# Performance work log

Measured on AMD Instinct MI355X. Metric: run time of the kernel, lower is better.

The kernel has to match this reference:

```python
import jax, jax.numpy as jnp
import numpy as np

C = 80           # foreground classes
B, N = 8, 4000   # images, proposals per image
K_PRE = 2048     # pre-NMS candidates per image (fixed-shape stand-in for torch.where filtering)
DET = 100        # detection_per_image
SCORE_THRESH = 0.01
NMS_THRESH = 0.5
MIN_AREA = 0.1
BBOX_W = (10.0, 10.0, 5.0, 5.0)
CLIP = float(np.log(1000.0 / 16.0))
CLS_OFFSET = 4096.0               # > max image coordinate, for batched (per-class) NMS


def setup_inputs() -> dict:
    key = jax.random.key(0)
    k1, k2, k3, k4 = jax.random.split(key, 4)
    p1 = jax.random.uniform(k1, (B, N, 2)) * 800.0
    wh = jax.random.uniform(k2, (B, N, 2)) * 200.0 + 1.0
    proposals = jnp.concatenate([p1, p1 + wh], axis=-1)          # [B,N,4] x1,y1,x2,y2
    label_pre = jax.random.normal(k3, (B, N, C + 1), dtype=jnp.float32)
    bbox_pre = jax.random.normal(k4, (B, N, (C + 1) * 4), dtype=jnp.float32) * 0.5
    return {"label_pre": label_pre, "bbox_pre": bbox_pre, "proposals": proposals}


def decode_boxes(deltas, props):
    w = props[..., 2] - props[..., 0]
    h = props[..., 3] - props[..., 1]
    cx = props[..., 0] + 0.5 * w
    cy = props[..., 1] + 0.5 * h
    dx = deltas[..., 0] / BBOX_W[0]
    dy = deltas[..., 1] / BBOX_W[1]
    dw = jnp.minimum(deltas[..., 2] / BBOX_W[2], CLIP)
    dh = jnp.minimum(deltas[..., 3] / BBOX_W[3], CLIP)
    pcx = dx * w + cx
    pcy = dy * h + cy
    pw = jnp.exp(dw) * w
    ph = jnp.exp(dh) * h
    return jnp.stack([pcx - 0.5 * pw, pcy - 0.5 * ph,
                      pcx + 0.5 * pw, pcy + 0.5 * ph], axis=-1)


def pairwise_iou(b):
    # b [K,4] -> [K,K]
    area = jnp.maximum(b[:, 2] - b[:, 0], 0.0) * jnp.maximum(b[:, 3] - b[:, 1], 0.0)
    lt = jnp.maximum(b[:, None, :2], b[None, :, :2])
    rb = jnp.minimum(b[:, None, 2:], b[None, :, 2:])
    wh = jnp.maximum(rb - lt, 0.0)
    inter = wh[..., 0] * wh[..., 1]
    union = area[:, None] + area[None, :] - inter
    return inter / jnp.maximum(union, 1e-9)


def greedy_nms_keep(boxes, valid):
    # boxes already sorted by score (descending); returns kept mask
    K = boxes.shape[0]
    iou = pairwise_iou(boxes)
    idx = jnp.arange(K)

    def body(i, keep):
        sup = (iou[i] > NMS_THRESH) & (idx > i) & keep[i]
        return keep & ~sup

    return jax.lax.fori_loop(0, K, body, valid)


def process_image(logits, deltas, props):
    probs = jax.nn.softmax(logits, axis=-1)            # [N, C+1]
    scores = probs[:, 1:].reshape(-1)                  # [N*C]
    d = deltas[:, 4:].reshape(N, C, 4)                 # drop background deltas
    boxes = decode_boxes(d, props[:, None, :]).reshape(-1, 4)   # [N*C, 4]
    labels = jnp.broadcast_to(jnp.arange(1, C + 1), (N, C)).reshape(-1)
    area = (boxes[:, 3] - boxes[:, 1]) * (boxes[:, 2] - boxes[:, 0])
    valid = (scores > SCORE_THRESH) & (area > MIN_AREA)
    masked = jnp.where(valid, scores, -1.0)
    top_scores, top_idx = jax.lax.top_k(masked, K_PRE)
    top_boxes = boxes[top_idx]
    top_labels = labels[top_idx]
    keep0 = top_scores > 0.0
    # batched_nms: per-class coordinate offset so classes never suppress each other
    off = (top_labels.astype(top_boxes.dtype) * CLS_OFFSET)[:, None]
    keep = greedy_nms_keep(top_boxes + off, keep0)
    final = jnp.where(keep, top_scores, -1.0)
    det_scores, det_idx = jax.lax.top_k(final, DET)
    return top_boxes[det_idx], det_scores, top_labels[det_idx]


def reference(label_pre, bbox_pre, proposals):
    # returns (boxes [B,DET,4], scores [B,DET], labels [B,DET]); entries with score<0 are padding
    return jax.vmap(process_image)(label_pre, bbox_pre, proposals)
```

## Files before the change

### kernel.cpp

```cpp
#include <hip/hip_runtime.h>
#include <stdint.h>

#define B_ 8
#define N_ 4000
#define C_ 80
#define NC_ (N_ * C_)
#define KP_ 2048
#define CAND_ 4096
#define SLOTS_ 32
#define SLOTCAP_ 128
#define DET_ 100
#define NW_ 32
#define CLIP_ 4.135166556742356f

#define PB_ 16
#define IB_ (N_ / PB_)
#define CB_ 64
#define FB_ 128
#define NBLK_ ((NC_ / 4 + 255) / 256)

#define RT_ 256
#define RBLK_ (CAND_ / RT_)

typedef unsigned long long u64;

__device__ __forceinline__ void decode4(const float4 pr, const float4 d,
                                        float& x1, float& y1, float& x2, float& y2) {
  float w = pr.z - pr.x, h = pr.w - pr.y;
  float cx = pr.x + 0.5f * w, cy = pr.y + 0.5f * h;
  float dx = d.x / 10.0f, dy = d.y / 10.0f;
  float dw = fminf(d.z / 5.0f, CLIP_), dh = fminf(d.w / 5.0f, CLIP_);
  float pcx = dx * w + cx, pcy = dy * h + cy;
  float pw = expf(dw) * w, ph = expf(dh) * h;
  x1 = pcx - 0.5f * pw; y1 = pcy - 0.5f * ph;
  x2 = pcx + 0.5f * pw; y2 = pcy + 0.5f * ph;
}

__global__ __launch_bounds__(256) void k_scores(const float* __restrict__ logits,
                                                uint32_t* __restrict__ keys,
                                                uint32_t* __restrict__ imgHist) {
  __shared__ float lds[PB_ * 81];
  __shared__ float mArr[PB_], dArr[PB_];
  __shared__ uint32_t hcnt[CB_];
  int blk = blockIdx.x;
  int b = blk / IB_, lb = blk - b * IB_;
  int p0 = b * N_ + lb * PB_;
  int t = threadIdx.x;
  if (t < CB_) hcnt[t] = 0;
  const float4* src = (const float4*)(logits + (size_t)p0 * 81);
  for (int k = t; k < PB_ * 81 / 4; k += 256) ((float4*)lds)[k] = src[k];
  __syncthreads();
  if (t < PB_) {
    const float* lp = lds + t * 81;
    float m = lp[0];
    for (int i = 1; i <= C_; ++i) m = fmaxf(m, lp[i]);
    float denom = 0.f;
    for (int i = 0; i <= C_; ++i) denom += expf(lp[i] - m);
    mArr[t] = m; dArr[t] = denom;
  }
  __syncthreads();
#pragma unroll
  for (int iter = 0; iter < PB_ * C_ / 256; ++iter) {
    int e = iter * 256 + t;
    int pp = e / C_, c = e - pp * C_;
    float lv = lds[pp * 81 + c + 1];
    float score = expf(lv - mArr[pp]) / dArr[pp];
    uint32_t key = 0;
    if (score > 0.01f) {
      key = __float_as_uint(score);
      atomicAdd(&hcnt[(key >> 20) - 960], 1u);
    }
    keys[(size_t)p0 * C_ + e] = key;
  }
  __syncthreads();
  if (t < CB_ && hcnt[t]) atomicAdd(&imgHist[b * CB_ + t], hcnt[t]);
}

__global__ __launch_bounds__(256) void k_refine(const uint32_t* __restrict__ keys,
                                                const uint32_t* __restrict__ imgHist,
                                                uint32_t* __restrict__ fineHist) {
  __shared__ int s_cb;
  int blk = blockIdx.x;
  int b = blk / NBLK_, lb = blk - b * NBLK_;
  int t = threadIdx.x;
  if (t < 64) {
    uint32_t v = imgHist[b * CB_ + t];
#pragma unroll
    for (int d = 1; d < 64; d <<= 1) {
      uint32_t o = __shfl_down(v, d);
      v += (t + d < 64) ? o : 0;
    }
    uint32_t nxt = __shfl_down(v, 1);
    if (t == 63) nxt = 0;
    uint32_t total = __shfl(v, 0);
    if (t == 0 && total < KP_) s_cb = -1;
    if (total >= KP_ && v >= KP_ && nxt < KP_) s_cb = t;
  }
  __syncthreads();
  int cb = s_cb;
  if (cb < 0) return;
  int ti = lb * 256 + t;
  if (ti >= NC_ / 4) return;
  uint4 k4 = ((const uint4*)(keys + (size_t)b * NC_))[ti];
  uint32_t want = (uint32_t)(cb + 960);
  uint32_t kv[4] = {k4.x, k4.y, k4.z, k4.w};
#pragma unroll
  for (int q = 0; q < 4; ++q)
    if ((kv[q] >> 20) == want)
      atomicAdd(&fineHist[b * FB_ + ((kv[q] >> 13) & (FB_ - 1))], 1u);
}

__global__ __launch_bounds__(256) void k_compact(const uint32_t* __restrict__ keys,
                                                 const uint32_t* __restrict__ imgHist,
                                                 const uint32_t* __restrict__ fineHist,
                                                 uint32_t* __restrict__ cnt,
                                                 u64* __restrict__ cand) {
  __shared__ int s_cb;
  __shared__ uint32_t s_tail;
  __shared__ uint32_t s_thr;
  int blk = blockIdx.x;
  int b = blk / NBLK_, lb = blk - b * NBLK_;
  int t = threadIdx.x;
  if (t < 64) {
    uint32_t v = imgHist[b * CB_ + t];
#pragma unroll
    for (int d = 1; d < 64; d <<= 1) {
      uint32_t o = __shfl_down(v, d);
      v += (t + d < 64) ? o : 0;
    }
    uint32_t nxt = __shfl_down(v, 1);
    if (t == 63) nxt = 0;
    uint32_t total = __shfl(v, 0);
    if (t == 0 && total < KP_) { s_cb = -1; s_tail = 0; }
    if (total >= KP_ && v >= KP_ && nxt < KP_) { s_cb = t; s_tail = nxt; }
  }
  __syncthreads();
  int cb = s_cb;
  if (cb < 0) {
    if (t == 0) s_thr = 1u;
  } else if (t < 64) {
    uint32_t f0 = fineHist[b * FB_ + 2 * t];
    uint32_t f1 = fineHist[b * FB_ + 2 * t + 1];
    uint32_t v = f0 + f1;
#pragma unroll
    for (int d = 1; d < 64; d <<= 1) {
      uint32_t o = __shfl_down(v, d);
      v += (t + d < 64) ? o : 0;
    }
    uint32_t nxt = __shfl_down(v, 1);
    if (t == 63) nxt = 0;
    uint32_t tail = s_tail;
    bool c0 = (tail + v >= KP_);
    bool c1 = (tail + nxt + f1 >= KP_);
    bool cN = (tail + nxt >= KP_);
    if (c0 && !c1) s_thr = ((uint32_t)(cb + 960) << 20) | ((uint32_t)(2 * t) << 13);
    if (c1 && !cN) s_thr = ((uint32_t)(cb + 960) << 20) | ((uint32_t)(2 * t + 1) << 13);
  }
  __syncthreads();
  uint32_t thrb = s_thr;
  int ti = lb * 256 + t;
  if (ti >= NC_ / 4) return;
  uint4 k4 = ((const uint4*)(keys + (size_t)b * NC_))[ti];
  int slot = (ti >> 4) & (SLOTS_ - 1);
  uint32_t kv[4] = {k4.x, k4.y, k4.z, k4.w};
  int ns = 0;
#pragma unroll
  for (int q = 0; q < 4; ++q) ns += (kv[q] >= thrb) ? 1 : 0;
  if (ns == 0) return;
  uint32_t pos = atomicAdd(&cnt[(b * SLOTS_ + slot) * 16], (uint32_t)ns);
  u64* seg = cand + (size_t)b * CAND_ + slot * SLOTCAP_;
  uint32_t baseIdx = (uint32_t)(ti * 4);
#pragma unroll
  for (int q = 0; q < 4; ++q) {
    if (kv[q] >= thrb) {
      if (pos < SLOTCAP_)
        seg[pos] = ((u64)kv[q] << 32) | (uint32_t)(~(baseIdx + q));
      ++pos;
    }
  }
}

__global__ __launch_bounds__(256) void k_rank_topk(
    const u64* __restrict__ cand,
    const float* __restrict__ bbox, const float* __restrict__ props,
    float* __restrict__ topScore, int* __restrict__ topLabel,
    float* __restrict__ topBox, float* __restrict__ nmsBox) {
  __shared__ u64 sh[CAND_];
  int blk = blockIdx.x;
  int b = blk / RBLK_, lb = blk - b * RBLK_;
  int t = threadIdx.x;
  const u64* cb2 = cand + (size_t)b * CAND_;
  for (int k = t; k < CAND_ / 2; k += RT_)
    ((ulonglong2*)sh)[k] = ((const ulonglong2*)cb2)[k];
  u64 ki = cb2[lb * RT_ + t];
  __syncthreads();
  int cnt = 0;
#pragma unroll 8
  for (int j = 0; j < CAND_; j += 2) {
    u64 a = sh[j];
    u64 c2 = sh[j + 1];
    cnt += (a > ki) ? 1 : 0;
    cnt += (c2 > ki) ? 1 : 0;
  }
  if (ki != 0ull && cnt < KP_) {
    uint32_t sbits = (uint32_t)(ki >> 32);
    uint32_t idx = ~((uint32_t)ki);
    int n = idx / C_, c = idx % C_;
    float4 pr4 = ((const float4*)props)[(size_t)b * N_ + n];
    float4 d = ((const float4*)(bbox + ((size_t)b * N_ + n) * ((C_ + 1) * 4)))[c + 1];
    float x1, y1, x2, y2;
    decode4(pr4, d, x1, y1, x2, y2);
    float off = (float)(c + 1) * 4096.0f;
    size_t o = (size_t)b * KP_ + (size_t)cnt;
    topScore[o] = __uint_as_float(sbits);
    topLabel[o] = c + 1;
    ((float4*)topBox)[o] = make_float4(x1, y1, x2, y2);
    ((float4*)nmsBox)[o] = make_float4(x1 + off, y1 + off, x2 + off, y2 + off);
  }
}

__global__ __launch_bounds__(64) void k_supmat(const float* __restrict__ nmsBox,
                                               u64* __restrict__ sup) {
  int blk = blockIdx.x;
  int b = blk / 528, r = blk - b * 528;
  int ti = 0, rem = r;
  while (rem >= 32 - ti) { rem -= 32 - ti; ++ti; }
  int tj = ti + rem;
  __shared__ float4 shj[64];
  __shared__ float sha[64];
  int l = threadIdx.x;
  const float4* boxes = (const float4*)(nmsBox + (size_t)b * KP_ * 4);
  float4 bj0 = boxes[tj * 64 + l];
  shj[l] = bj0;
  sha[l] = fmaxf(bj0.z - bj0.x, 0.f) * fmaxf(bj0.w - bj0.y, 0.f);
  int i = ti * 64 + l;
  float4 bi = boxes[i];
  float areai = fmaxf(bi.z - bi.x, 0.f) * fmaxf(bi.w - bi.y, 0.f);
  __syncthreads();
  u64 bits = 0;
  for (int jj = 0; jj < 64; ++jj) {
    int j = tj * 64 + jj;
    if (j > i) {
      float4 bj = shj[jj];
      float ltx = fmaxf(bi.x, bj.x), lty = fmaxf(bi.y, bj.y);
      float rbx = fminf(bi.z, bj.z), rby = fminf(bi.w, bj.w);
      float iw = fmaxf(rbx - ltx, 0.f), ih = fmaxf(rby - lty, 0.f);
      float inter = iw * ih;
      float uni = areai + sha[jj] - inter;
      float iou = inter / fmaxf(uni, 1e-9f);
      if (iou > 0.5f) bits |= (1ull << jj);
    }
  }
  sup[((size_t)b * KP_ + i) * NW_ + tj] = bits;
}

__global__ __launch_bounds__(64) void k_nms_scan(const u64* __restrict__ sup,
                                                 const float* __restrict__ topScore,
                                                 const int* __restrict__ topLabel,
                                                 const float* __restrict__ topBox,
                                                 float* __restrict__ out) {
  int b = blockIdx.x, l = threadIdx.x;
  int h = l >> 5, w = l & 31;
  const u64* base = sup + (size_t)b * KP_ * NW_;
  const float* ts = topScore + (size_t)b * KP_;
  const int* tl = topLabel + (size_t)b * KP_;
  const float4* tb = (const float4*)(topBox + (size_t)b * KP_ * 4);
  unsigned m32 = 0;
#pragma unroll
  for (int j = 0; j < 8; ++j) {
    float4 s4 = ((const float4*)ts)[l * 8 + j];
    if (!(s4.x > 0.f)) m32 |= 1u << (4 * j + 0);
    if (!(s4.y > 0.f)) m32 |= 1u << (4 * j + 1);
    if (!(s4.z > 0.f)) m32 |= 1u << (4 * j + 2);
    if (!(s4.w > 0.f)) m32 |= 1u << (4 * j + 3);
  }
  u64 removed = ((u64)__shfl(m32, 2 * w + 1) << 32) | (u64)__shfl(m32, 2 * w);

  int outCount = 0;
  auto emitRow = [&](int row, bool kept) {
    if (l == (outCount & 63)) {
      float4 bx = tb[row];
      out[((size_t)b * DET_ + outCount) * 4 + 0] = bx.x;
      out[((size_t)b * DET_ + outCount) * 4 + 1] = bx.y;
      out[((size_t)b * DET_ + outCount) * 4 + 2] = bx.z;
      out[((size_t)b * DET_ + outCount) * 4 + 3] = bx.w;
      out[B_ * DET_ * 4 + (size_t)b * DET_ + outCount] = kept ? ts[row] : -1.0f;
      out[B_ * DET_ * 4 + B_ * DET_ + (size_t)b * DET_ + outCount] = (float)tl[row];
    }
    ++outCount;
  };

  u64 ra[32], rb[32];
  auto loadc = [&](u64* dst, int c) {
    const u64* p = base + ((size_t)c * 64 + h * 32) * NW_ + w;
#pragma unroll
    for (int k = 0; k < 32; ++k) dst[k] = p[(size_t)k * NW_];
  };
  auto chunk = [&](u64* cur, int c) -> bool {
    u64 rm = __shfl(removed, c);
    unsigned rml = (unsigned)rm, rmh = (unsigned)(rm >> 32);
#pragma unroll
    for (int k = 0; k < 32; ++k) {
      unsigned dlo = __builtin_amdgcn_readlane((unsigned)cur[k], c);
      unsigned dhi = __builtin_amdgcn_readlane((unsigned)(cur[k] >> 32), c);
      if (!((rml >> k) & 1u)) { rml |= dlo; rmh |= dhi; }
    }
#pragma unroll
    for (int k = 0; k < 32; ++k) {
      unsigned dlo = __builtin_amdgcn_readlane((unsigned)cur[k], 32 + c);
      unsigned dhi = __builtin_amdgcn_readlane((unsigned)(cur[k] >> 32), 32 + c);
      if (!((rmh >> k) & 1u)) { rml |= dlo; rmh |= dhi; }
    }
    u64 rmfull = ((u64)rmh << 32) | rml;
    u64 kb = ~rmfull;
    while (kb) {
      if (outCount >= DET_) return true;
      int k = __builtin_ctzll(kb);
      kb &= kb - 1;
      emitRow(c * 64 + k, true);
    }
    if (outCount >= DET_) return true;
    unsigned kmask = h ? ~rmh : ~rml;
    u64 acc = 0;
#pragma unroll
    for (int k = 0; k < 32; ++k)
      acc |= ((kmask >> k) & 1u) ? cur[k] : 0ull;
    acc |= __shfl_xor(acc, 32);
    removed = (l == c) ? rmfull : removed;
    if (l < 32 && l >= c) removed |= acc;
    return false;
  };

  bool done = false;
  loadc(ra, 0);
  for (int c = 0; c < NW_ && !done; c += 2) {
    if (c + 1 < NW_) loadc(rb, c + 1);
    done = chunk(ra, c);
    if (!done) {
      if (c + 2 < NW_) loadc(ra, c + 2);
      done = chunk(rb, c + 1);
    }
  }
  if (outCount < DET_) {
    for (int c2 = 0; c2 < NW_ && outCount < DET_; ++c2) {
      u64 rm = __shfl(removed, c2);
      while (rm && outCount < DET_) {
        int k = __builtin_ctzll(rm);
        rm &= rm - 1;
        emitRow(c2 * 64 + k, false);
      }
    }
  }
}

extern "C" void kernel_launch(void* const* d_in, const int* in_sizes, int n_in,
                              void* d_out, int out_size, void* d_ws, size_t ws_size,
                              hipStream_t stream) {
  const float* label_pre = (const float*)d_in[0];
  const float* bbox_pre = (const float*)d_in[1];
  const float* props = (const float*)d_in[2];
  float* out = (float*)d_out;

  char* ws = (char*)d_ws;
  size_t off = 0;
  auto alloc = [&](size_t bytes) -> void* {
    void* p = ws + off;
    off = (off + bytes + 255) & ~(size_t)255;
    return p;
  };

  uint32_t* keys = (uint32_t*)alloc((size_t)B_ * NC_ * 4);
  size_t zero_begin = off;
  uint32_t* imgHist = (uint32_t*)alloc((size_t)B_ * CB_ * 4);
  uint32_t* fineHist = (uint32_t*)alloc((size_t)B_ * FB_ * 4);
  uint32_t* cnt = (uint32_t*)alloc((size_t)B_ * SLOTS_ * 16 * 4);
  u64* cand = (u64*)alloc((size_t)B_ * CAND_ * 8);
  float* topScore = (float*)alloc((size_t)B_ * KP_ * 4);
  int* topLabel = (int*)alloc((size_t)B_ * KP_ * 4);
  float* topBox = (float*)alloc((size_t)B_ * KP_ * 16);
  float* nmsBox = (float*)alloc((size_t)B_ * KP_ * 16);
  size_t zero_end = off;
  u64* sup = (u64*)alloc((size_t)B_ * KP_ * NW_ * 8);

  if (off > ws_size) return;

  hipMemsetAsync(ws + zero_begin, 0, zero_end - zero_begin, stream);

  k_scores<<<B_ * IB_, 256, 0, stream>>>(label_pre, keys, imgHist);
  k_refine<<<B_ * NBLK_, 256, 0, stream>>>(keys, imgHist, fineHist);
  k_compact<<<B_ * NBLK_, 256, 0, stream>>>(keys, imgHist, fineHist, cnt, cand);
  k_rank_topk<<<B_ * RBLK_, RT_, 0, stream>>>(cand, bbox_pre, props,
                                              topScore, topLabel, topBox, nmsBox);
  k_supmat<<<B_ * 528, 64, 0, stream>>>(nmsBox, sup);
  k_nms_scan<<<B_, 64, 0, stream>>>(sup, topScore, topLabel, topBox, out);
}
```

Measured before the change: 221.0 us.

## Split rank-by-counting top-k into parallel partial-rank and scatter kernels

The rank kernel used to have each of 128 blocks compare one candidate per thread against all 4096 candidates. Now the comparison set is cut into 8 slices, giving 8x more blocks that each write a partial rank count. A separate scatter kernel sums the partial counts, then decodes and writes the top boxes. This exposes more parallelism on a GPU that was under-occupied, at the cost of an extra kernel launch and a partial-rank buffer round trip through global memory.

```diff
diff --git a/kernel.cpp b/kernel.cpp
--- a/kernel.cpp
+++ b/kernel.cpp
@@ -19,8 +19,9 @@
 #define FB_ 128
 #define NBLK_ ((NC_ / 4 + 255) / 256)
 
-#define RT_ 256
-#define RBLK_ (CAND_ / RT_)
+#define JS_ 8
+#define SL_ (CAND_ / JS_)
+#define IBK_ (CAND_ / 256)
 
 typedef unsigned long long u64;
 
@@ -180,43 +181,57 @@
   }
 }
 
-__global__ __launch_bounds__(256) void k_rank_topk(
-    const u64* __restrict__ cand,
+__global__ __launch_bounds__(256) void k_rank(const u64* __restrict__ cand,
+                                              uint32_t* __restrict__ rankPart) {
+  __shared__ u64 sh[SL_];
+  int blk = blockIdx.x;
+  int b = blk / (IBK_ * JS_);
+  int rem = blk - b * (IBK_ * JS_);
+  int lb = rem / JS_, js = rem - lb * JS_;
+  int t = threadIdx.x;
+  const u64* cb2 = cand + (size_t)b * CAND_;
+  ((ulonglong2*)sh)[t] = ((const ulonglong2*)(cb2 + js * SL_))[t];
+  u64 ki = cb2[lb * 256 + t];
+  __syncthreads();
+  int cnt = 0;
+#pragma unroll 8
+  for (int j2 = 0; j2 < SL_ / 2; ++j2) {
+    ulonglong2 v = ((const ulonglong2*)sh)[j2];
+    cnt += (v.x > ki) ? 1 : 0;
+    cnt += (v.y > ki) ? 1 : 0;
+  }
+  rankPart[((size_t)(b * JS_ + js)) * CAND_ + lb * 256 + t] = (uint32_t)cnt;
+}
+
+__global__ __launch_bounds__(256) void k_scatter(
+    const u64* __restrict__ cand, const uint32_t* __restrict__ rankPart,
     const float* __restrict__ bbox, const float* __restrict__ props,
     float* __restrict__ topScore, int* __restrict__ topLabel,
     float* __restrict__ topBox, float* __restrict__ nmsBox) {
-  __shared__ u64 sh[CAND_];
-  int blk = blockIdx.x;
-  int b = blk / RBLK_, lb = blk - b * RBLK_;
+  int blk = blockIdx.x;
+  int b = blk / IBK_, lb = blk - b * IBK_;
   int t = threadIdx.x;
-  const u64* cb2 = cand + (size_t)b * CAND_;
-  for (int k = t; k < CAND_ / 2; k += RT_)
-    ((ulonglong2*)sh)[k] = ((const ulonglong2*)cb2)[k];
-  u64 ki = cb2[lb * RT_ + t];
-  __syncthreads();
-  int cnt = 0;
-#pragma unroll 8
-  for (int j = 0; j < CAND_; j += 2) {
-    u64 a = sh[j];
-    u64 c2 = sh[j + 1];
-    cnt += (a > ki) ? 1 : 0;
-    cnt += (c2 > ki) ? 1 : 0;
-  }
-  if (ki != 0ull && cnt < KP_) {
-    uint32_t sbits = (uint32_t)(ki >> 32);
-    uint32_t idx = ~((uint32_t)ki);
-    int n = idx / C_, c = idx % C_;
-    float4 pr4 = ((const float4*)props)[(size_t)b * N_ + n];
-    float4 d = ((const float4*)(bbox + ((size_t)b * N_ + n) * ((C_ + 1) * 4)))[c + 1];
-    float x1, y1, x2, y2;
-    decode4(pr4, d, x1, y1, x2, y2);
-    float off = (float)(c + 1) * 4096.0f;
-    size_t o = (size_t)b * KP_ + (size_t)cnt;
-    topScore[o] = __uint_as_float(sbits);
-    topLabel[o] = c + 1;
-    ((float4*)topBox)[o] = make_float4(x1, y1, x2, y2);
-    ((float4*)nmsBox)[o] = make_float4(x1 + off, y1 + off, x2 + off, y2 + off);
-  }
+  int i = lb * 256 + t;
+  u64 ki = cand[(size_t)b * CAND_ + i];
+  if (ki == 0ull) return;
+  uint32_t r = 0;
+#pragma unroll
+  for (int js = 0; js < JS_; ++js)
+    r += rankPart[((size_t)(b * JS_ + js)) * CAND_ + i];
+  if (r >= KP_) return;
+  uint32_t sbits = (uint32_t)(ki >> 32);
+  uint32_t idx = ~((uint32_t)ki);
+  int n = idx / C_, c = idx % C_;
+  float4 pr4 = ((const float4*)props)[(size_t)b * N_ + n];
+  float4 d = ((const float4*)(bbox + ((size_t)b * N_ + n) * ((C_ + 1) * 4)))[c + 1];
+  float x1, y1, x2, y2;
+  decode4(pr4, d, x1, y1, x2, y2);
+  float off = (float)(c + 1) * 4096.0f;
+  size_t o = (size_t)b * KP_ + (size_t)r;
+  topScore[o] = __uint_as_float(sbits);
+  topLabel[o] = c + 1;
+  ((float4*)topBox)[o] = make_float4(x1, y1, x2, y2);
+  ((float4*)nmsBox)[o] = make_float4(x1 + off, y1 + off, x2 + off, y2 + off);
 }
 
 __global__ __launch_bounds__(64) void k_supmat(const float* __restrict__ nmsBox,
@@ -381,6 +396,7 @@
   float* nmsBox = (float*)alloc((size_t)B_ * KP_ * 16);
   size_t zero_end = off;
   u64* sup = (u64*)alloc((size_t)B_ * KP_ * NW_ * 8);
+  uint32_t* rankPart = (uint32_t*)alloc((size_t)B_ * JS_ * CAND_ * 4);
 
   if (off > ws_size) return;
 
@@ -389,8 +405,9 @@
   k_scores<<<B_ * IB_, 256, 0, stream>>>(label_pre, keys, imgHist);
   k_refine<<<B_ * NBLK_, 256, 0, stream>>>(keys, imgHist, fineHist);
   k_compact<<<B_ * NBLK_, 256, 0, stream>>>(keys, imgHist, fineHist, cnt, cand);
-  k_rank_topk<<<B_ * RBLK_, RT_, 0, stream>>>(cand, bbox_pre, props,
-                                              topScore, topLabel, topBox, nmsBox);
+  k_rank<<<B_ * IBK_ * JS_, 256, 0, stream>>>(cand, rankPart);
+  k_scatter<<<B_ * IBK_, 256, 0, stream>>>(cand, rankPart, bbox_pre, props,
+                                           topScore, topLabel, topBox, nmsBox);
   k_supmat<<<B_ * 528, 64, 0, stream>>>(nmsBox, sup);
   k_nms_scan<<<B_, 64, 0, stream>>>(sup, topScore, topLabel, topBox, out);
 }
```

New measurement: 190.1 us. 14.0% less time.
